# Kernel tuning notes

Measured on AMD Instinct MI355X. Metric: run time of the kernel, lower is better.

The kernel has to match this reference:

```python
import jax, jax.numpy as jnp
import numpy as np

N, D = 8192, 4096
DIM_K = 4096

def setup_inputs() -> dict:
    key0 = jax.random.key(0)
    k1, k2, k3 = jax.random.split(key0, 3)
    return {
        "query": jax.random.normal(k1, (N, D), dtype=jnp.float32),
        "key": jax.random.normal(k2, (D, N), dtype=jnp.float32),
        "value": jax.random.normal(k3, (N, D), dtype=jnp.float32),
    }

def reference(query, key, value):
    # Faithful to the (buggy) torch module: ELEMENTWISE query * key.T,
    # scale by sqrt(dim_k), elementwise * value, softmax over dim=1
    # (F.softmax's implicit dim for a 2D tensor). The mask branch in the
    # original (`if x:`) cannot execute for multi-element tensors, so it
    # is omitted (mask=None path).
    scale = jnp.sqrt(jnp.float32(DIM_K))
    x = (query * key.T) / scale  # [N, D]
    x = x * value                # [N, D]
    return jax.nn.softmax(x, axis=1)
```

## Files before the change

### kernel.cpp

```cpp
#include <hip/hip_runtime.h>
#include <math.h>


static constexpr int NROW = 8192;
static constexpr int D    = 4096;
static constexpr float SCL = 0.015625f;

__device__ __forceinline__ unsigned short f2bf(float f) {
    unsigned int b = __float_as_uint(f);
    b = (b + 0x7FFFu + ((b >> 16) & 1u)) >> 16;
    return (unsigned short)b;
}
__device__ __forceinline__ float bf2f(unsigned short u) {
    return __uint_as_float(((unsigned int)u) << 16);
}

__global__ __launch_bounds__(256, 4)
void kt_transpose_kernel(const float* __restrict__ K,
                         unsigned short* __restrict__ KT)
{
    __shared__ float lds[64][129];
    const int t  = threadIdx.x;
    const int jt = blockIdx.x & 63;
    const int it = blockIdx.x >> 6;
    const int j0 = jt * 64;
    const int i0 = it * 128;

    const int i4 = t & 31;
    const int jb = t >> 5;
    #pragma unroll
    for (int s = 0; s < 8; ++s) {
        const int jr = s * 8 + jb;
        const float4 v =
            *(const float4*)(K + (size_t)(j0 + jr) * NROW + i0 + 4 * i4);
        *(float4*)&lds[jr][4 * i4] = v;
    }
    __syncthreads();

    const int j4 = t & 15;
    const int ib = t >> 4;
    #pragma unroll
    for (int sw = 0; sw < 8; ++sw) {
        const int il = sw * 16 + ib;
        ushort4 w;
        w.x = f2bf(lds[4 * j4 + 0][il]);
        w.y = f2bf(lds[4 * j4 + 1][il]);
        w.z = f2bf(lds[4 * j4 + 2][il]);
        w.w = f2bf(lds[4 * j4 + 3][il]);
        *(ushort4*)(KT + (size_t)(i0 + il) * D + j0 + 4 * j4) = w;
    }
}

__global__ __launch_bounds__(256, 6)
void sdp_stream_kernel(const float* __restrict__ Q,
                       const unsigned short* __restrict__ KT,
                       const float* __restrict__ V,
                       float* __restrict__ O)
{
    __shared__ float ssum[4];

    const int tid  = threadIdx.x;
    const int wv   = tid >> 6;
    const int lane = tid & 63;
    const int r    = blockIdx.x * 2 + (wv >> 1);
    const int hbase = (wv & 1) * 2048;

    const float*          qrow = Q  + (size_t)r * D + hbase;
    const unsigned short* krow = KT + (size_t)r * D + hbase;
    const float*          vrow = V  + (size_t)r * D + hbase;
    float*                orow = O  + (size_t)r * D + hbase;
    const int c0 = 4 * lane;

    float4  qA = *(const float4*)(qrow + 0 * 256 + c0);
    ushort4 kA = *(const ushort4*)(krow + 0 * 256 + c0);
    float4  vA = *(const float4*)(vrow + 0 * 256 + c0);
    float4  qB = *(const float4*)(qrow + 1 * 256 + c0);
    ushort4 kB = *(const ushort4*)(krow + 1 * 256 + c0);
    float4  vB = *(const float4*)(vrow + 1 * 256 + c0);
    float4  qC = *(const float4*)(qrow + 2 * 256 + c0);
    ushort4 kC = *(const ushort4*)(krow + 2 * 256 + c0);
    float4  vC = *(const float4*)(vrow + 2 * 256 + c0);
    float4  qD = *(const float4*)(qrow + 3 * 256 + c0);
    ushort4 kD = *(const ushort4*)(krow + 3 * 256 + c0);
    float4  vD = *(const float4*)(vrow + 3 * 256 + c0);

    ushort4 e0, e1, e2, e3, e4, e5, e6, e7;
    float s = 0.0f;

#define BODY(t, ET, QS, KS, VS)                                               \
    {                                                                         \
        const float4 qc = QS; const ushort4 kc = KS; const float4 vc = VS;    \
        if ((t) + 4 < 8) {                                                    \
            QS = *(const float4*)(qrow + ((t) + 4) * 256 + c0);               \
            KS = *(const ushort4*)(krow + ((t) + 4) * 256 + c0);              \
            VS = *(const float4*)(vrow + ((t) + 4) * 256 + c0);               \
        }                                                                     \
        const float ex = __expf(((qc.x * bf2f(kc.x)) * SCL) * vc.x);          \
        const float ey = __expf(((qc.y * bf2f(kc.y)) * SCL) * vc.y);          \
        const float ez = __expf(((qc.z * bf2f(kc.z)) * SCL) * vc.z);          \
        const float ew = __expf(((qc.w * bf2f(kc.w)) * SCL) * vc.w);          \
        s += ((ex + ey) + (ez + ew));                                         \
        ET.x = f2bf(ex); ET.y = f2bf(ey); ET.z = f2bf(ez); ET.w = f2bf(ew);   \
        __builtin_amdgcn_sched_barrier(0);                                    \
    }

    BODY(0, e0, qA, kA, vA)
    BODY(1, e1, qB, kB, vB)
    BODY(2, e2, qC, kC, vC)
    BODY(3, e3, qD, kD, vD)
    BODY(4, e4, qA, kA, vA)
    BODY(5, e5, qB, kB, vB)
    BODY(6, e6, qC, kC, vC)
    BODY(7, e7, qD, kD, vD)
#undef BODY

    #pragma unroll
    for (int i = 1; i < 64; i <<= 1)
        s += __shfl_xor(s, i, 64);
    if (lane == 0) ssum[wv] = s;
    __syncthreads();
    const float inv = 1.0f / (ssum[wv] + ssum[wv ^ 1]);

#define WRITE_TILE(t, ET)                                                     \
    {                                                                         \
        float4 xx;                                                            \
        xx.x = bf2f(ET.x) * inv;                                              \
        xx.y = bf2f(ET.y) * inv;                                              \
        xx.z = bf2f(ET.z) * inv;                                              \
        xx.w = bf2f(ET.w) * inv;                                              \
        *(float4*)(orow + (size_t)(t) * 256 + c0) = xx;                       \
    }

    WRITE_TILE(0, e0)  WRITE_TILE(1, e1)  WRITE_TILE(2, e2)  WRITE_TILE(3, e3)
    WRITE_TILE(4, e4)  WRITE_TILE(5, e5)  WRITE_TILE(6, e6)  WRITE_TILE(7, e7)
#undef WRITE_TILE
}

extern "C" void kernel_launch(void* const* d_in, const int* in_sizes, int n_in,
                              void* d_out, int out_size, void* d_ws, size_t ws_size,
                              hipStream_t stream) {
    const float* Q = (const float*)d_in[0];
    const float* K = (const float*)d_in[1];
    const float* V = (const float*)d_in[2];
    float* O = (float*)d_out;

    unsigned short* KT = (unsigned short*)d_ws;
    kt_transpose_kernel<<<dim3(64 * 64), dim3(256), 0, stream>>>(K, KT);
    sdp_stream_kernel<<<dim3(NROW / 2), dim3(256), 0, stream>>>(Q, KT, V, O);
}
```

Before: 133.1 us.

## Assign one row per block with four waves splitting the row

```diff
diff --git a/kernel.cpp b/kernel.cpp
--- a/kernel.cpp
+++ b/kernel.cpp
@@ -62,56 +62,45 @@
     const int tid  = threadIdx.x;
     const int wv   = tid >> 6;
     const int lane = tid & 63;
-    const int r    = blockIdx.x * 2 + (wv >> 1);
-    const int hbase = (wv & 1) * 2048;
+    const int r    = blockIdx.x;
+    const int base = wv * 1024;
 
-    const float*          qrow = Q  + (size_t)r * D + hbase;
-    const unsigned short* krow = KT + (size_t)r * D + hbase;
-    const float*          vrow = V  + (size_t)r * D + hbase;
-    float*                orow = O  + (size_t)r * D + hbase;
+    const float*          qrow = Q  + (size_t)r * D + base;
+    const unsigned short* krow = KT + (size_t)r * D + base;
+    const float*          vrow = V  + (size_t)r * D + base;
+    float*                orow = O  + (size_t)r * D + base;
     const int c0 = 4 * lane;
 
-    float4  qA = *(const float4*)(qrow + 0 * 256 + c0);
-    ushort4 kA = *(const ushort4*)(krow + 0 * 256 + c0);
-    float4  vA = *(const float4*)(vrow + 0 * 256 + c0);
-    float4  qB = *(const float4*)(qrow + 1 * 256 + c0);
-    ushort4 kB = *(const ushort4*)(krow + 1 * 256 + c0);
-    float4  vB = *(const float4*)(vrow + 1 * 256 + c0);
-    float4  qC = *(const float4*)(qrow + 2 * 256 + c0);
-    ushort4 kC = *(const ushort4*)(krow + 2 * 256 + c0);
-    float4  vC = *(const float4*)(vrow + 2 * 256 + c0);
-    float4  qD = *(const float4*)(qrow + 3 * 256 + c0);
-    ushort4 kD = *(const ushort4*)(krow + 3 * 256 + c0);
-    float4  vD = *(const float4*)(vrow + 3 * 256 + c0);
+    float4  q0 = *(const float4*)(qrow + 0 * 256 + c0);
+    ushort4 k0 = *(const ushort4*)(krow + 0 * 256 + c0);
+    float4  v0 = *(const float4*)(vrow + 0 * 256 + c0);
+    float4  q1 = *(const float4*)(qrow + 1 * 256 + c0);
+    ushort4 k1 = *(const ushort4*)(krow + 1 * 256 + c0);
+    float4  v1 = *(const float4*)(vrow + 1 * 256 + c0);
+    float4  q2 = *(const float4*)(qrow + 2 * 256 + c0);
+    ushort4 k2 = *(const ushort4*)(krow + 2 * 256 + c0);
+    float4  v2 = *(const float4*)(vrow + 2 * 256 + c0);
+    float4  q3 = *(const float4*)(qrow + 3 * 256 + c0);
+    ushort4 k3 = *(const ushort4*)(krow + 3 * 256 + c0);
+    float4  v3 = *(const float4*)(vrow + 3 * 256 + c0);
 
-    ushort4 e0, e1, e2, e3, e4, e5, e6, e7;
+    ushort4 e0, e1, e2, e3;
     float s = 0.0f;
 
-#define BODY(t, ET, QS, KS, VS)                                               \
+#define BODY(ET, QS, KS, VS)                                                  \
     {                                                                         \
-        const float4 qc = QS; const ushort4 kc = KS; const float4 vc = VS;    \
-        if ((t) + 4 < 8) {                                                    \
-            QS = *(const float4*)(qrow + ((t) + 4) * 256 + c0);               \
-            KS = *(const ushort4*)(krow + ((t) + 4) * 256 + c0);              \
-            VS = *(const float4*)(vrow + ((t) + 4) * 256 + c0);               \
-        }                                                                     \
-        const float ex = __expf(((qc.x * bf2f(kc.x)) * SCL) * vc.x);          \
-        const float ey = __expf(((qc.y * bf2f(kc.y)) * SCL) * vc.y);          \
-        const float ez = __expf(((qc.z * bf2f(kc.z)) * SCL) * vc.z);          \
-        const float ew = __expf(((qc.w * bf2f(kc.w)) * SCL) * vc.w);          \
+        const float ex = __expf(((QS.x * bf2f(KS.x)) * SCL) * VS.x);          \
+        const float ey = __expf(((QS.y * bf2f(KS.y)) * SCL) * VS.y);          \
+        const float ez = __expf(((QS.z * bf2f(KS.z)) * SCL) * VS.z);          \
+        const float ew = __expf(((QS.w * bf2f(KS.w)) * SCL) * VS.w);          \
         s += ((ex + ey) + (ez + ew));                                         \
         ET.x = f2bf(ex); ET.y = f2bf(ey); ET.z = f2bf(ez); ET.w = f2bf(ew);   \
-        __builtin_amdgcn_sched_barrier(0);                                    \
     }
 
-    BODY(0, e0, qA, kA, vA)
-    BODY(1, e1, qB, kB, vB)
-    BODY(2, e2, qC, kC, vC)
-    BODY(3, e3, qD, kD, vD)
-    BODY(4, e4, qA, kA, vA)
-    BODY(5, e5, qB, kB, vB)
-    BODY(6, e6, qC, kC, vC)
-    BODY(7, e7, qD, kD, vD)
+    BODY(e0, q0, k0, v0)
+    BODY(e1, q1, k1, v1)
+    BODY(e2, q2, k2, v2)
+    BODY(e3, q3, k3, v3)
 #undef BODY
 
     #pragma unroll
@@ -119,7 +108,7 @@
         s += __shfl_xor(s, i, 64);
     if (lane == 0) ssum[wv] = s;
     __syncthreads();
-    const float inv = 1.0f / (ssum[wv] + ssum[wv ^ 1]);
+    const float inv = 1.0f / (((ssum[0] + ssum[1]) + (ssum[2] + ssum[3])));
 
 #define WRITE_TILE(t, ET)                                                     \
     {                                                                         \
@@ -132,7 +121,6 @@
     }
 
     WRITE_TILE(0, e0)  WRITE_TILE(1, e1)  WRITE_TILE(2, e2)  WRITE_TILE(3, e3)
-    WRITE_TILE(4, e4)  WRITE_TILE(5, e5)  WRITE_TILE(6, e6)  WRITE_TILE(7, e7)
 #undef WRITE_TILE
 }
 
@@ -146,5 +134,5 @@
 
     unsigned short* KT = (unsigned short*)d_ws;
     kt_transpose_kernel<<<dim3(64 * 64), dim3(256), 0, stream>>>(K, KT);
-    sdp_stream_kernel<<<dim3(NROW / 2), dim3(256), 0, stream>>>(Q, KT, V, O);
+    sdp_stream_kernel<<<dim3(NROW), dim3(256), 0, stream>>>(Q, KT, V, O);
 }
```

Result: faster. 128.7 us (-3.3%).
